# Optimization experiments

Measured on AMD Instinct MI355X. Metric: run time of the kernel, lower is better.

## Reference

```python
import jax, jax.numpy as jnp
import numpy as np

B, S, D = 2, 4096, 2048
HQ, HK, HV = 32, 8, 8
H = max(HQ, HK, HV)
DK, DV = 64, 64
OUT = 2048
CHUNK = 64  # chunked-recurrent block size


def setup_inputs() -> dict:
    key = jax.random.key(0)
    k1, k2, k3 = jax.random.split(key, 3)
    x = jax.random.normal(k1, (B, S, D), dtype=jnp.float32)
    input_state = jnp.zeros((B, H * DK * DV), dtype=jnp.float32)
    qkv = HQ * DK + HK * DK + HV * DV  # 3072
    # Linear weights stored as [in, out]; equals torch weight.T so y = x @ W
    W_in = jax.random.normal(k2, (D, qkv), dtype=jnp.float32) * (D ** -0.5)
    W_out = jax.random.normal(k3, (H * DV, OUT), dtype=jnp.float32) * ((H * DV) ** -0.5)
    return {"x": x, "input_state": input_state, "W_in": W_in, "W_out": W_out}


def _linear_attention(q, k, v, S0):
    # q,k,v: [B,S,H,d]; S0: [B,H,DK,DV]
    nc = S // CHUNK
    # move chunk axis to front for lax.scan: [nc, B, CHUNK, H, d]
    qc = jnp.moveaxis(q.reshape(B, nc, CHUNK, H, DK), 1, 0)
    kc = jnp.moveaxis(k.reshape(B, nc, CHUNK, H, DK), 1, 0)
    vc = jnp.moveaxis(v.reshape(B, nc, CHUNK, H, DV), 1, 0)
    mask = jnp.tril(jnp.ones((CHUNK, CHUNK), dtype=bool))  # causal within chunk

    def step(Sstate, blk):
        qb, kb, vb = blk  # [B,C,H,d]
        A = jnp.einsum('bihd,bjhd->bhij', qb, kb)
        A = jnp.where(mask, A, jnp.zeros((), A.dtype))
        o = jnp.einsum('bhij,bjhd->bihd', A, vb) \
            + jnp.einsum('bihd,bhde->bihe', qb, Sstate)
        Sstate = Sstate + jnp.einsum('bjhd,bjhe->bhde', kb, vb)
        return Sstate, o

    Sf, o = jax.lax.scan(step, S0, (qc, kc, vc))
    o = jnp.moveaxis(o, 0, 1).reshape(B, S, H, DV)
    return o, Sf


def reference(x, input_state, W_in, W_out):
    proj = x @ W_in  # [B,S,3072]
    q, k, v = jnp.split(proj, [HQ * DK, HQ * DK + HK * DK], axis=-1)
    q = q.reshape(B, S, HQ, DK)
    k = k.reshape(B, S, HK, DK)
    v = v.reshape(B, S, HV, DV)
    # GQA: repeat kv heads up to num_heads = max(...)
    k = jnp.repeat(k, H // HK, axis=2)
    v = jnp.repeat(v, H // HV, axis=2)
    S0 = input_state.reshape(B, H, DK, DV)
    o, Sf = _linear_attention(q, k, v, S0)
    out = o.reshape(B, S, H * DV) @ W_out
    return out, Sf.reshape(B, H, DK * DV)
```

## Files before the change

### kernel.cpp

```cpp
#include <hip/hip_runtime.h>

typedef __bf16 bf16_t;
typedef __bf16 bf16x8 __attribute__((ext_vector_type(8)));
typedef __bf16 bf16x4 __attribute__((ext_vector_type(4)));
typedef float  f32x4  __attribute__((ext_vector_type(4)));

#define MFMA16(a,b,c) __builtin_amdgcn_mfma_f32_16x16x32_bf16((a),(b),(c),0,0,0)

__device__ __forceinline__ void gl_lds16(const void* g, void* l) {
    __builtin_amdgcn_global_load_lds(
        (__attribute__((address_space(1))) void*)(g),
        (__attribute__((address_space(3))) void*)(l),
        16, 0, 0);
}

static constexpr int S_TOT   = 8192;
static constexpr int D_IN    = 2048;
static constexpr int QKV     = 3072;
static constexpr int OUT_D   = 2048;
static constexpr int NCHUNK  = 64;
static constexpr int ZSTR    = 88;

__global__ __launch_bounds__(256)
void prep(const float* __restrict__ x, bf16_t* __restrict__ xb,
          const float* __restrict__ W_in, bf16_t* __restrict__ WinT,
          const float* __restrict__ W_out, bf16_t* __restrict__ WoutT) {
    __shared__ float tile[64][65];
    const int bid = blockIdx.x;
    const int t   = threadIdx.x;
    if (bid < 16384) {
        int i = bid * 256 + t;
        f32x4 v = ((const f32x4*)x)[i];
        bf16x4 o;
        o[0] = (bf16_t)v[0]; o[1] = (bf16_t)v[1]; o[2] = (bf16_t)v[2]; o[3] = (bf16_t)v[3];
        ((bf16x4*)xb)[i] = o;
        return;
    }
    const float* in; bf16_t* out; int R, C, bx, by;
    int tb = bid - 16384;
    if (tb < 1536) { in = W_in;  out = WinT;  R = 2048; C = 3072; bx = tb % 48; by = tb / 48; }
    else { tb -= 1536; in = W_out; out = WoutT; R = 2048; C = 2048; bx = tb % 32; by = tb / 32; }
    const int r0 = by * 64, c0 = bx * 64;
#pragma unroll
    for (int p = 0; p < 4; p++) {
        int row = p * 16 + (t >> 4);
        int col = (t & 15) * 4;
        f32x4 v = *(const f32x4*)&in[(size_t)(r0 + row) * C + c0 + col];
        tile[row][col + 0] = v[0]; tile[row][col + 1] = v[1];
        tile[row][col + 2] = v[2]; tile[row][col + 3] = v[3];
    }
    __syncthreads();
#pragma unroll
    for (int p = 0; p < 4; p++) {
        int oc  = p * 16 + (t >> 4);
        int orr = (t & 15) * 4;
        bf16x4 v;
        v[0] = (bf16_t)tile[orr + 0][oc]; v[1] = (bf16_t)tile[orr + 1][oc];
        v[2] = (bf16_t)tile[orr + 2][oc]; v[3] = (bf16_t)tile[orr + 3][oc];
        *(bf16x4*)&out[(size_t)(c0 + oc) * R + r0 + orr] = v;
    }
}

template<int OUT_BF16>
__global__ __launch_bounds__(256, 4)
void gemm_bt(const bf16_t* __restrict__ A, const bf16_t* __restrict__ Bt,
             void* __restrict__ Cout, int M, int N, int K) {
    __shared__ alignas(16) bf16_t lA[128 * 64];
    __shared__ alignas(16) bf16_t lB[128 * 64];
    const int tid = threadIdx.x;
    const int m0 = blockIdx.y * 128;
    const int n0 = blockIdx.x * 128;
    const int w = tid >> 6, lane = tid & 63;
    const int wr = (w >> 1) * 64, wc = (w & 1) * 64;
    const int l15 = lane & 15, q = lane >> 4, q4 = q * 4;
    const int trow = tid >> 3;
    const int tcc  = (tid & 7) ^ (trow & 7);
    const bf16_t* Ag = A + (size_t)(m0 + trow) * K + tcc * 8;
    const bf16_t* Bg = Bt + (size_t)(n0 + trow) * K + tcc * 8;
    bf16_t* lA_t = lA + tid * 8;
    bf16_t* lB_t = lB + tid * 8;
    const size_t rs = (size_t)32 * K;
    const int cc0 = (q)     ^ (l15 & 7);
    const int cc1 = (4 + q) ^ (l15 & 7);
    f32x4 acc[4][4] = {};
    for (int k0 = 0; k0 < K; k0 += 64) {
#pragma unroll
        for (int j = 0; j < 4; j++) {
            gl_lds16(Ag + k0 + j * rs, lA_t + j * 2048);
            gl_lds16(Bg + k0 + j * rs, lB_t + j * 2048);
        }
        __syncthreads();
#pragma unroll
        for (int ksub = 0; ksub < 2; ksub++) {
            const int cc = ksub ? cc1 : cc0;
            bf16x8 bfr[4];
#pragma unroll
            for (int nj = 0; nj < 4; nj++)
                bfr[nj] = *(const bf16x8*)&lB[(wc + nj * 16 + l15) * 64 + cc * 8];
#pragma unroll
            for (int mi = 0; mi < 4; mi++) {
                bf16x8 afr = *(const bf16x8*)&lA[(wr + mi * 16 + l15) * 64 + cc * 8];
#pragma unroll
                for (int nj = 0; nj < 4; nj++)
                    acc[mi][nj] = MFMA16(afr, bfr[nj], acc[mi][nj]);
            }
        }
        __syncthreads();
    }
    if (OUT_BF16) {
        bf16_t* C = (bf16_t*)Cout;
#pragma unroll
        for (int mi = 0; mi < 4; mi++)
#pragma unroll
            for (int nj = 0; nj < 4; nj++)
#pragma unroll
                for (int r = 0; r < 4; r++)
                    C[(size_t)(m0 + wr + mi * 16 + q4 + r) * N + n0 + wc + nj * 16 + l15] =
                        (bf16_t)acc[mi][nj][r];
    } else {
        float* C = (float*)Cout;
#pragma unroll
        for (int mi = 0; mi < 4; mi++)
#pragma unroll
            for (int nj = 0; nj < 4; nj++)
#pragma unroll
                for (int r = 0; r < 4; r++)
                    C[(size_t)(m0 + wr + mi * 16 + q4 + r) * N + n0 + wc + nj * 16 + l15] =
                        acc[mi][nj][r];
    }
}

__global__ __launch_bounds__(64)
void kv_fused(const bf16_t* __restrict__ proj, bf16_t* __restrict__ vT_g,
              float* __restrict__ Zc) {
    const int idx = blockIdx.x;
    const int c = idx & 63, hk = (idx >> 6) & 7, b = idx >> 9;
    const int tokBase = b * 4096 + c * 64;
    __shared__ float tk[64][65];
    __shared__ float tv[64][65];
    const int lane = threadIdx.x;
    const bf16_t* kg = proj + (size_t)tokBase * QKV + 2048 + hk * 64;
    const bf16_t* vg = proj + (size_t)tokBase * QKV + 2560 + hk * 64;
#pragma unroll
    for (int p = 0; p < 8; p++) {
        int tok = p * 8 + (lane >> 3);
        int d0  = (lane & 7) * 8;
        bf16x8 kv = *(const bf16x8*)&kg[(size_t)tok * QKV + d0];
        bf16x8 vv = *(const bf16x8*)&vg[(size_t)tok * QKV + d0];
#pragma unroll
        for (int e = 0; e < 8; e++) {
            tk[tok][d0 + e] = (float)kv[e];
            tv[tok][d0 + e] = (float)vv[e];
        }
    }
    __syncthreads();
#pragma unroll
    for (int p = 0; p < 8; p++) {
        int dv = p * 8 + (lane >> 3);
        int t0 = (lane & 7) * 8;
        bf16x8 o;
#pragma unroll
        for (int e = 0; e < 8; e++) o[e] = (bf16_t)tv[t0 + e][dv];
        *(bf16x8*)&vT_g[(size_t)idx * 4096 + dv * 64 + t0] = o;
    }
    const int l15 = lane & 15, q8 = (lane >> 4) * 8, q4 = (lane >> 4) * 4;
    f32x4 acc[4][4] = {};
#pragma unroll
    for (int ks = 0; ks < 2; ks++) {
        bf16x8 af[4], bf_[4];
#pragma unroll
        for (int mi = 0; mi < 4; mi++)
#pragma unroll
            for (int e = 0; e < 8; e++) af[mi][e] = (bf16_t)tv[ks * 32 + q8 + e][mi * 16 + l15];
#pragma unroll
        for (int nj = 0; nj < 4; nj++)
#pragma unroll
            for (int e = 0; e < 8; e++) bf_[nj][e] = (bf16_t)tk[ks * 32 + q8 + e][nj * 16 + l15];
#pragma unroll
        for (int mi = 0; mi < 4; mi++)
#pragma unroll
            for (int nj = 0; nj < 4; nj++)
                acc[mi][nj] = MFMA16(af[mi], bf_[nj], acc[mi][nj]);
    }
    float* zout = Zc + (size_t)idx * 4096;
#pragma unroll
    for (int mi = 0; mi < 4; mi++)
#pragma unroll
        for (int nj = 0; nj < 4; nj++)
#pragma unroll
            for (int r = 0; r < 4; r++)
                zout[(mi * 16 + q4 + r) * 64 + nj * 16 + l15] = acc[mi][nj][r];
}

__global__ __launch_bounds__(256)
void prefix_state(const float* __restrict__ Zc, const float* __restrict__ S0,
                  bf16_t* __restrict__ Zp, float* __restrict__ SfOut) {
    const int slice = blockIdx.x & 15;
    const int bh = blockIdx.x >> 4;
    const int h = bh & 31, b = bh >> 5;
    const int hk = h >> 2;
    const int e = slice * 256 + threadIdx.x;
    const int dv = e >> 6, dk = e & 63;
    float acc = S0[(size_t)b * 131072 + h * 4096 + dk * 64 + dv];
    const float* zc = Zc + ((size_t)(b * 8 + hk) * 64) * 4096 + e;
    bf16_t* zp = Zp + ((size_t)(b * 32 + h) * 64) * 4096 + e;
#pragma unroll 4
    for (int c = 0; c < NCHUNK; c++) {
        zp[(size_t)c * 4096] = (bf16_t)acc;
        acc += zc[(size_t)c * 4096];
    }
    SfOut[(size_t)b * 131072 + h * 4096 + dk * 64 + dv] = acc;
}

__global__ __launch_bounds__(256)
void attn_chunk(const bf16_t* __restrict__ proj, const bf16_t* __restrict__ vT_g,
                const bf16_t* __restrict__ Zp, bf16_t* __restrict__ O) {
    const int idx = blockIdx.x;
    const int hk = idx & 7, c = (idx >> 3) & 63, b = idx >> 9;
    const int g = threadIdx.x >> 6, lane = threadIdx.x & 63;
    const int h = hk * 4 + g;
    const int tokBase = b * 4096 + c * 64;
    __shared__ alignas(16) bf16_t zs_all[4][64 * ZSTR];
    bf16_t* zs = zs_all[g];
    const int l15 = lane & 15, q8 = (lane >> 4) * 8, q4 = (lane >> 4) * 4;
    const bf16_t* qrow  = proj + (size_t)tokBase * QKV + h * 64;
    const bf16_t* krow  = proj + (size_t)tokBase * QKV + 2048 + hk * 64;
    const bf16_t* zrow  = Zp + (((size_t)(b * 32 + h)) * 64 + c) * 4096;
    const bf16_t* vTrow = vT_g + ((size_t)(b * 8 + hk) * 64 + c) * 4096;

    bf16x8 qf[2][4];
#pragma unroll
    for (int ks = 0; ks < 2; ks++)
#pragma unroll
        for (int mi = 0; mi < 4; mi++)
            qf[ks][mi] = *(const bf16x8*)&qrow[(size_t)(mi * 16 + l15) * QKV + ks * 32 + q8];

    f32x4 oacc[4][4] = {};
#pragma unroll
    for (int ks = 0; ks < 2; ks++) {
        bf16x8 zf[4];
#pragma unroll
        for (int nj = 0; nj < 4; nj++) zf[nj] = *(const bf16x8*)&zrow[(nj * 16 + l15) * 64 + ks * 32 + q8];
#pragma unroll
        for (int mi = 0; mi < 4; mi++)
#pragma unroll
            for (int nj = 0; nj < 4; nj++)
                oacc[mi][nj] = MFMA16(qf[ks][mi], zf[nj], oacc[mi][nj]);
    }
    f32x4 sacc[4][4] = {};
#pragma unroll
    for (int ks = 0; ks < 2; ks++) {
        bf16x8 kf[4];
#pragma unroll
        for (int nj = 0; nj < 4; nj++) kf[nj] = *(const bf16x8*)&krow[(size_t)(nj * 16 + l15) * QKV + ks * 32 + q8];
#pragma unroll
        for (int mi = 0; mi < 4; mi++)
#pragma unroll
            for (int nj = 0; nj < 4; nj++)
                if (mi >= nj) sacc[mi][nj] = MFMA16(qf[ks][mi], kf[nj], sacc[mi][nj]);
    }
#pragma unroll
    for (int mi = 0; mi < 4; mi++)
#pragma unroll
        for (int nj = 0; nj < 4; nj++)
#pragma unroll
            for (int r = 0; r < 4; r++) {
                int ti = mi * 16 + q4 + r, tj = nj * 16 + l15;
                float v = (ti >= tj) ? sacc[mi][nj][r] : 0.0f;
                zs[ti * ZSTR + tj] = (bf16_t)v;
            }
    __syncthreads();
#pragma unroll
    for (int ks = 0; ks < 2; ks++) {
        bf16x8 sf[4], vf[4];
#pragma unroll
        for (int mi = 0; mi < 4; mi++) sf[mi] = *(const bf16x8*)&zs[(mi * 16 + l15) * ZSTR + ks * 32 + q8];
#pragma unroll
        for (int nj = 0; nj < 4; nj++) vf[nj] = *(const bf16x8*)&vTrow[(nj * 16 + l15) * 64 + ks * 32 + q8];
#pragma unroll
        for (int mi = 0; mi < 4; mi++)
#pragma unroll
            for (int nj = 0; nj < 4; nj++)
                oacc[mi][nj] = MFMA16(sf[mi], vf[nj], oacc[mi][nj]);
    }
    bf16_t* og = O + (size_t)tokBase * OUT_D + h * 64;
#pragma unroll
    for (int mi = 0; mi < 4; mi++)
#pragma unroll
        for (int nj = 0; nj < 4; nj++)
#pragma unroll
            for (int r = 0; r < 4; r++)
                og[(size_t)(mi * 16 + q4 + r) * OUT_D + nj * 16 + l15] = (bf16_t)oacc[mi][nj][r];
}

extern "C" void kernel_launch(void* const* d_in, const int* in_sizes, int n_in,
                              void* d_out, int out_size, void* d_ws, size_t ws_size,
                              hipStream_t stream) {
    const float* x     = (const float*)d_in[0];
    const float* S0    = (const float*)d_in[1];
    const float* W_in  = (const float*)d_in[2];
    const float* W_out = (const float*)d_in[3];

    char* ws = (char*)d_ws;
    bf16_t* xb    = (bf16_t*)(ws + 0);
    bf16_t* WinT  = (bf16_t*)(ws + 33554432);
    bf16_t* WoutT = (bf16_t*)(ws + 46137344);
    bf16_t* proj  = (bf16_t*)(ws + 54525952);
    float*  Zc    = (float*) (ws + 104857600);
    bf16_t* Zp    = (bf16_t*)(ws + 121634816);
    bf16_t* vT_g  = (bf16_t*)(ws + 0);
    bf16_t* Ob    = (bf16_t*)(ws + 8388608);

    float* outMain  = (float*)d_out;
    float* outState = (float*)d_out + (size_t)S_TOT * OUT_D;

    prep<<<16384 + 1536 + 1024, 256, 0, stream>>>(x, xb, W_in, WinT, W_out, WoutT);
    gemm_bt<1><<<dim3(24, 64), 256, 0, stream>>>(xb, WinT, proj, S_TOT, QKV, D_IN);
    kv_fused<<<1024, 64, 0, stream>>>(proj, vT_g, Zc);
    prefix_state<<<1024, 256, 0, stream>>>(Zc, S0, Zp, outState);
    attn_chunk<<<1024, 256, 0, stream>>>(proj, vT_g, Zp, Ob);
    gemm_bt<0><<<dim3(16, 64), 256, 0, stream>>>(Ob, WoutT, outMain, S_TOT, OUT_D, OUT_D);
}
```

Before: 371.2 us.

## Double-buffer A tile in LDS and stream B fragments straight into registers

The GEMM kernel now keeps two LDS buffers for the A tile and prefetches the next K-slice asynchronously while computing the current one, which needs only one barrier per iteration. The B operand no longer goes through LDS: each lane loads its MFMA fragments directly from global memory into registers, and the next slice is prefetched after the MFMAs. This aims to cut barrier stalls and LDS traffic. In exchange it raises register pressure and duplicates B global reads across the two waves that share a column block, and the B prefetch has little compute after it to hide its latency.

```diff
diff --git a/kernel.cpp b/kernel.cpp
--- a/kernel.cpp
+++ b/kernel.cpp
@@ -65,47 +65,57 @@
 __global__ __launch_bounds__(256, 4)
 void gemm_bt(const bf16_t* __restrict__ A, const bf16_t* __restrict__ Bt,
              void* __restrict__ Cout, int M, int N, int K) {
-    __shared__ alignas(16) bf16_t lA[128 * 64];
-    __shared__ alignas(16) bf16_t lB[128 * 64];
+    __shared__ alignas(16) bf16_t lA[2][128 * 64];
     const int tid = threadIdx.x;
     const int m0 = blockIdx.y * 128;
     const int n0 = blockIdx.x * 128;
     const int w = tid >> 6, lane = tid & 63;
     const int wr = (w >> 1) * 64, wc = (w & 1) * 64;
-    const int l15 = lane & 15, q = lane >> 4, q4 = q * 4;
+    const int l15 = lane & 15, q = lane >> 4, q4 = q * 4, q8 = q * 8;
     const int trow = tid >> 3;
     const int tcc  = (tid & 7) ^ (trow & 7);
     const bf16_t* Ag = A + (size_t)(m0 + trow) * K + tcc * 8;
-    const bf16_t* Bg = Bt + (size_t)(n0 + trow) * K + tcc * 8;
-    bf16_t* lA_t = lA + tid * 8;
-    bf16_t* lB_t = lB + tid * 8;
-    const size_t rs = (size_t)32 * K;
-    const int cc0 = (q)     ^ (l15 & 7);
+    const bf16_t* Bg = Bt + (size_t)(n0 + wc + l15) * K + q8;
+    const size_t rs  = (size_t)32 * K;
+    const size_t njs = (size_t)16 * K;
+    const int cc0 = q ^ (l15 & 7);
     const int cc1 = (4 + q) ^ (l15 & 7);
     f32x4 acc[4][4] = {};
+    bf16x8 breg[2][4];
+#pragma unroll
+    for (int j = 0; j < 4; j++)
+        gl_lds16(Ag + j * rs, &lA[0][tid * 8 + j * 2048]);
+#pragma unroll
+    for (int ks = 0; ks < 2; ks++)
+#pragma unroll
+        for (int nj = 0; nj < 4; nj++)
+            breg[ks][nj] = *(const bf16x8*)(Bg + nj * njs + ks * 32);
     for (int k0 = 0; k0 < K; k0 += 64) {
-#pragma unroll
-        for (int j = 0; j < 4; j++) {
-            gl_lds16(Ag + k0 + j * rs, lA_t + j * 2048);
-            gl_lds16(Bg + k0 + j * rs, lB_t + j * 2048);
+        const int cur = (k0 >> 6) & 1;
+        __syncthreads();
+        if (k0 + 64 < K) {
+#pragma unroll
+            for (int j = 0; j < 4; j++)
+                gl_lds16(Ag + k0 + 64 + j * rs, &lA[cur ^ 1][tid * 8 + j * 2048]);
         }
-        __syncthreads();
 #pragma unroll
         for (int ksub = 0; ksub < 2; ksub++) {
             const int cc = ksub ? cc1 : cc0;
-            bf16x8 bfr[4];
-#pragma unroll
-            for (int nj = 0; nj < 4; nj++)
-                bfr[nj] = *(const bf16x8*)&lB[(wc + nj * 16 + l15) * 64 + cc * 8];
 #pragma unroll
             for (int mi = 0; mi < 4; mi++) {
-                bf16x8 afr = *(const bf16x8*)&lA[(wr + mi * 16 + l15) * 64 + cc * 8];
+                bf16x8 afr = *(const bf16x8*)&lA[cur][(wr + mi * 16 + l15) * 64 + cc * 8];
 #pragma unroll
                 for (int nj = 0; nj < 4; nj++)
-                    acc[mi][nj] = MFMA16(afr, bfr[nj], acc[mi][nj]);
+                    acc[mi][nj] = MFMA16(afr, breg[ksub][nj], acc[mi][nj]);
             }
         }
-        __syncthreads();
+        if (k0 + 64 < K) {
+#pragma unroll
+            for (int ks = 0; ks < 2; ks++)
+#pragma unroll
+                for (int nj = 0; nj < 4; nj++)
+                    breg[ks][nj] = *(const bf16x8*)(Bg + k0 + 64 + nj * njs + ks * 32);
+        }
     }
     if (OUT_BF16) {
         bf16_t* C = (bf16_t*)Cout;
```

After: 539.3 us. 1.45x slower.
